# Kernel optimization log

Measured on AMD Instinct MI355X. Metric: run time of the kernel, lower is better.

The kernel has to match this reference:

```python
import jax, jax.numpy as jnp
import numpy as np

EPS = 1e-6
SIGMA = 0.1  # temperature for pseudo-LBS blend weights


def _quat_rotate(q, v):
    # q: [..., 4] (w, x, y, z) unit quaternions, v: [..., 3]
    qw, qv = q[..., :1], q[..., 1:]
    t = 2.0 * jnp.cross(qv, v)
    return v + qw * t + jnp.cross(qv, t)


def _pairwise_sqdist(a, b):
    # a: [n, d], b: [m, d] -> [n, m]
    return (jnp.sum(a * a, -1, keepdims=True)
            + jnp.sum(b * b, -1)[None, :]
            - 2.0 * (a @ b.T))


def setup_inputs() -> dict:
    N, K, F, V, J, P, M, H = 300000, 80, 64, 6890, 24, 64, 64, 128
    key = jax.random.key(0)
    ks = jax.random.split(key, 16)
    s = lambda i, shape: jax.random.normal(ks[i], shape, dtype=jnp.float32) * 0.05
    return {
        "xyz": jax.random.normal(ks[0], (N, 3), dtype=jnp.float32),
        "feature": jax.random.normal(ks[1], (N, F), dtype=jnp.float32),
        "centers": jax.random.normal(ks[2], (K, F), dtype=jnp.float32),
        "smpl_verts": jax.random.normal(ks[3], (V, 3), dtype=jnp.float32),
        "skinning_weights": jax.random.uniform(ks[4], (V, J), dtype=jnp.float32),
        "body_pose_feature": jax.random.normal(ks[5], (J, P), dtype=jnp.float32),
        "w_body": s(6, (P + F, M)),
        "b_body": jnp.zeros((M,), jnp.float32),
        "w_pos1": s(7, (3 + M, H)),
        "b_pos1": jnp.zeros((H,), jnp.float32),
        "w_pos2": s(8, (H, M)),
        "b_pos2": jnp.zeros((M,), jnp.float32),
        "w_rot": s(9, (M, 4)),
        "b_rot": jnp.zeros((4,), jnp.float32),
        "w_trans": s(10, (M, 3)),
        "b_trans": jnp.zeros((3,), jnp.float32),
    }


def reference(xyz, feature, centers, smpl_verts, skinning_weights,
              body_pose_feature, w_body, b_body, w_pos1, b_pos1,
              w_pos2, b_pos2, w_rot, b_rot, w_trans, b_trans):
    # ---- soft k-means: soft assignment of N points to K garment joints ----
    a = jax.nn.softmax(-_pairwise_sqdist(feature, centers), axis=-1)  # [N, K]
    cnt = a.sum(axis=0) + EPS                                          # [K]
    # weighted segment-reduce: c_assign^T @ xyz, diag(1/count) normalize
    joint_xyz = (a.T @ xyz) / cnt[:, None]      # [K, 3]
    joint_feat = (a.T @ feature) / cnt[:, None]  # [K, F] (cluster centers)

    # ---- KNN (k=1) skin-weight lookup against SMPL canonical verts ----
    idx = jnp.argmin(_pairwise_sqdist(joint_xyz, smpl_verts), axis=-1)  # [K]
    pts_W = skinning_weights[idx]                                        # [K, J]

    # ---- garment pose decoder ----
    body_feat = pts_W @ body_pose_feature                 # [K, P]
    g = jnp.concatenate([body_feat, joint_feat], axis=-1)  # [K, P+F]
    g = jax.nn.gelu(g @ w_body + b_body)                   # [K, M]
    lo, hi = smpl_verts.min(0), smpl_verts.max(0)
    xn = 2.0 * (joint_xyz - lo) / (hi - lo + EPS) - 1.0    # aabb sym-normalize
    h = jax.nn.relu(jnp.concatenate([xn, g], -1) @ w_pos1 + b_pos1)
    g2 = h @ w_pos2 + b_pos2                               # [K, M]
    q = g2 @ w_rot + b_rot
    q = q / (jnp.linalg.norm(q, axis=-1, keepdims=True) + EPS)  # [K, 4]
    t = g2 @ w_trans + b_trans                                   # [K, 3]

    # ---- pseudo-LBS: blend per-joint transforms back to N points ----
    w = jax.nn.softmax(-_pairwise_sqdist(xyz, joint_xyz) / SIGMA, axis=-1)  # [N, K]
    qb = w @ q
    qb = qb / (jnp.linalg.norm(qb, axis=-1, keepdims=True) + EPS)  # [N, 4]
    deformed_xyz = _quat_rotate(qb, xyz) + w @ t                    # [N, 3]
    return deformed_xyz
```

## Files before the change

### kernel.cpp

```cpp
#include <hip/hip_runtime.h>
#include <math.h>

#define N_PTS 300000
#define NJ 80
#define FDIM 64
#define VN 6890
#define NROUND 9375
#define GRID_A 256
#define TOTW 1024
#define SLOT_B 8704

typedef __attribute__((ext_vector_type(8))) short short8;
typedef __attribute__((ext_vector_type(4))) float f32x4;

union Frag { uint32_t u[4]; short8 v; };

__device__ __forceinline__ uint32_t packhi(float a, float b) {
  return (__float_as_uint(a) >> 16) | (__float_as_uint(b) & 0xFFFF0000u);
}
__device__ __forceinline__ uint32_t packlo(float a, float b) {
  float la = a - __uint_as_float(__float_as_uint(a) & 0xFFFF0000u);
  float lb = b - __uint_as_float(__float_as_uint(b) & 0xFFFF0000u);
  return packhi(la, lb);
}

#define DPPF(x, ctrl) __uint_as_float((uint32_t)__builtin_amdgcn_update_dpp( \
    0, (int)__float_as_uint(x), (ctrl), 0xF, 0xF, true))

__device__ __forceinline__ void gl16(const float* g, const void* l) {
  __builtin_amdgcn_global_load_lds(
      (const __attribute__((address_space(1))) void*)g,
      (__attribute__((address_space(3))) void*)l, 16, 0, 0);
}
__device__ __forceinline__ void gl4(const float* g, const void* l) {
  __builtin_amdgcn_global_load_lds(
      (const __attribute__((address_space(1))) void*)g,
      (__attribute__((address_space(3))) void*)l, 4, 0, 0);
}

__global__ __launch_bounds__(256, 2) void kA(
    const float* __restrict__ xyz, const float* __restrict__ feature,
    const float* __restrict__ centers, float* __restrict__ jacc,
    float* __restrict__ part)
{
  __shared__ __align__(16) unsigned char ring[4][3][SLOT_B];
  __shared__ ushort sChi[NJ][72];
  __shared__ ushort sClo[NJ][72];

  const int tid = threadIdx.x;
  const int w = tid >> 6;
  const int l = tid & 63;
  const int i = l & 15;
  const int g = l >> 4;
  const int gw = blockIdx.x * 4 + w;

  auto STAGE = [&](int st, int rs) {
    const float* fb = feature + (size_t)rs * 2048;
    unsigned char* base = &ring[w][st][0];
#pragma unroll
    for (int k = 0; k < 8; ++k) {
      const int lu = k * 64 + l;
      const int ptl = lu >> 4;
      const int gu = ptl * 16 + ((lu & 15) ^ (ptl & 7));
      gl16(fb + gu * 4, base + k * 1024);
    }
    const float* xb = xyz + (size_t)rs * 96;
#pragma unroll
    for (int k = 0; k < 2; ++k) {
      int fi = k * 64 + l; if (fi > 95) fi = 95;
      gl4(xb + fi, base + 8192 + k * 256);
    }
  };

  {
    int r1 = gw + TOTW; if (r1 > NROUND - 1) r1 = NROUND - 1;
    STAGE(0, gw);
    STAGE(1, r1);
  }

  for (int idx = tid; idx < NJ * FDIM; idx += 256) {
    float f = centers[idx];
    sChi[idx >> 6][idx & 63] = (ushort)(__float_as_uint(f) >> 16);
    float lo = f - __uint_as_float(__float_as_uint(f) & 0xFFFF0000u);
    sClo[idx >> 6][idx & 63] = (ushort)(__float_as_uint(lo) >> 16);
  }
  float cn[5];
#pragma unroll
  for (int nt = 0; nt < 5; ++nt) {
    float s = 0.f;
    const float* cp = centers + (size_t)(i + 16 * nt) * FDIM + 8 * g;
#pragma unroll
    for (int e = 0; e < 8; ++e) {
      float a0 = cp[e], a1 = cp[32 + e];
      s += a0 * a0 + a1 * a1;
    }
    s += __shfl_xor(s, 16);
    s += __shfl_xor(s, 32);
    cn[nt] = s;
  }
  __syncthreads();

  f32x4 acc2[5][5];
#pragma unroll
  for (int a = 0; a < 5; ++a)
#pragma unroll
    for (int b = 0; b < 5; ++b) acc2[a][b] = (f32x4){0.f, 0.f, 0.f, 0.f};

  int s3 = 0;
  for (int r = gw; r < NROUND; r += TOTW) {
    asm volatile("s_waitcnt vmcnt(10)" ::: "memory");
    __builtin_amdgcn_sched_barrier(0);
    {
      int rn = r + 2 * TOTW; if (rn > NROUND - 1) rn = NROUND - 1;
      int st = s3 + 2; if (st >= 3) st -= 3;
      STAGE(st, rn);
    }
    __builtin_amdgcn_sched_barrier(0);

    const float* F = (const float*)&ring[w][s3][0];
    const float* X = (const float*)&ring[w][s3][8192];

    Frag pA[5];
#pragma unroll
    for (int c = 0; c < 2; ++c) {
      f32x4 acc1[5];
#pragma unroll
      for (int nt = 0; nt < 5; ++nt) acc1[nt] = (f32x4){0.f, 0.f, 0.f, 0.f};

      const int ptl = 16 * c + i;
      const int m = ptl & 7;
#pragma unroll
      for (int ks = 0; ks < 2; ++ks) {
        const int j = 8 * ks + 2 * g;
        float4 va = *(const float4*)(F + ptl * 64 + ((j ^ m) << 2));
        float4 vb = *(const float4*)(F + ptl * 64 + (((j + 1) ^ m) << 2));
        Frag ah, al;
        ah.u[0] = packhi(va.x, va.y); ah.u[1] = packhi(va.z, va.w);
        ah.u[2] = packhi(vb.x, vb.y); ah.u[3] = packhi(vb.z, vb.w);
        al.u[0] = packlo(va.x, va.y); al.u[1] = packlo(va.z, va.w);
        al.u[2] = packlo(vb.x, vb.y); al.u[3] = packlo(vb.z, vb.w);
#pragma unroll
        for (int nt = 0; nt < 5; ++nt) {
          Frag bh, bl;
          *(uint4*)bh.u = *(const uint4*)&sChi[i + 16 * nt][32 * ks + 8 * g];
          *(uint4*)bl.u = *(const uint4*)&sClo[i + 16 * nt][32 * ks + 8 * g];
          acc1[nt] = __builtin_amdgcn_mfma_f32_16x16x32_bf16(ah.v, bh.v, acc1[nt], 0, 0, 0);
          acc1[nt] = __builtin_amdgcn_mfma_f32_16x16x32_bf16(al.v, bh.v, acc1[nt], 0, 0, 0);
          acc1[nt] = __builtin_amdgcn_mfma_f32_16x16x32_bf16(ah.v, bl.v, acc1[nt], 0, 0, 0);
        }
      }

      f32x4 e5[5];
#pragma unroll
      for (int nt = 0; nt < 5; ++nt)
#pragma unroll
        for (int rr = 0; rr < 4; ++rr) e5[nt][rr] = 2.f * acc1[nt][rr] - cn[nt];
      float rs[4];
#pragma unroll
      for (int rr = 0; rr < 4; ++rr) {
        float mm = e5[0][rr];
#pragma unroll
        for (int nt = 1; nt < 5; ++nt) mm = fmaxf(mm, e5[nt][rr]);
        mm = fmaxf(mm, DPPF(mm, 0xB1));
        mm = fmaxf(mm, DPPF(mm, 0x4E));
        mm = fmaxf(mm, DPPF(mm, 0x141));
        mm = fmaxf(mm, DPPF(mm, 0x140));
        float ss = 0.f;
#pragma unroll
        for (int nt = 0; nt < 5; ++nt) {
          float e = __expf(e5[nt][rr] - mm);
          e5[nt][rr] = e;
          ss += e;
        }
        ss += DPPF(ss, 0xB1);
        ss += DPPF(ss, 0x4E);
        ss += DPPF(ss, 0x141);
        ss += DPPF(ss, 0x140);
        rs[rr] = __builtin_amdgcn_rcpf(ss);
      }
#pragma unroll
      for (int nt = 0; nt < 5; ++nt) {
        pA[nt].u[2 * c + 0] = packhi(e5[nt][0] * rs[0], e5[nt][1] * rs[1]);
        pA[nt].u[2 * c + 1] = packhi(e5[nt][2] * rs[2], e5[nt][3] * rs[3]);
      }
    }

#pragma unroll
    for (int ct = 0; ct < 5; ++ct) {
      Frag B;
      float x[8];
      if (ct < 4) {
        const int d = 16 * ct + i, jd = d >> 2, db = d & 3;
#pragma unroll
        for (int n = 0; n < 8; ++n) {
          const int ptl = (n < 4) ? (4 * g + n) : (16 + 4 * g + (n - 4));
          x[n] = F[ptl * 64 + ((jd ^ (ptl & 7)) << 2) + db];
        }
      } else {
#pragma unroll
        for (int n = 0; n < 8; ++n) {
          const int ptl = (n < 4) ? (4 * g + n) : (16 + 4 * g + (n - 4));
          x[n] = (i < 3) ? X[ptl * 3 + i] : (i == 3 ? 1.f : 0.f);
        }
      }
      B.u[0] = packhi(x[0], x[1]); B.u[1] = packhi(x[2], x[3]);
      B.u[2] = packhi(x[4], x[5]); B.u[3] = packhi(x[6], x[7]);
#pragma unroll
      for (int nt = 0; nt < 5; ++nt)
        acc2[nt][ct] = __builtin_amdgcn_mfma_f32_16x16x32_bf16(pA[nt].v, B.v, acc2[nt][ct], 0, 0, 0);
    }

    s3 += 1; if (s3 >= 3) s3 -= 3;
  }

  asm volatile("s_waitcnt vmcnt(0)" ::: "memory");
  __syncthreads();
  float* sJ = (float*)&ring[0][0][0];
  for (int idx = tid; idx < 5440; idx += 256) sJ[idx] = 0.f;
  __syncthreads();
#pragma unroll
  for (int ww = 0; ww < 4; ++ww) {
    if (w == ww) {
#pragma unroll
      for (int nt = 0; nt < 5; ++nt)
#pragma unroll
        for (int ct = 0; ct < 5; ++ct) {
          if (ct < 4 || i < 4) {
            const int col = 16 * ct + i;
#pragma unroll
            for (int rr = 0; rr < 4; ++rr)
              sJ[(16 * nt + 4 * g + rr) * 68 + col] += acc2[nt][ct][rr];
          }
        }
    }
    __syncthreads();
  }
  if (part) {
    for (int idx = tid; idx < 5440; idx += 256)
      part[(size_t)blockIdx.x * 5440 + idx] = sJ[idx];
  } else {
    for (int idx = tid; idx < 5440; idx += 256)
      atomicAdd(&jacc[idx], sJ[idx]);
  }
}

__global__ __launch_bounds__(256) void kR(const float* __restrict__ part,
                                          float* __restrict__ jacc)
{
  const int bx = blockIdx.x;
  const int cg = bx % 22, sl = bx / 22;
  const int t = cg * 256 + threadIdx.x;
  if (t >= 5440) return;
  const int b0 = sl * (GRID_A / 16);
  float s0 = 0.f, s1 = 0.f, s2 = 0.f, s3 = 0.f;
  for (int b = b0; b < b0 + GRID_A / 16; b += 4) {
    s0 += part[(size_t)(b + 0) * 5440 + t];
    s1 += part[(size_t)(b + 1) * 5440 + t];
    s2 += part[(size_t)(b + 2) * 5440 + t];
    s3 += part[(size_t)(b + 3) * 5440 + t];
  }
  atomicAdd(&jacc[t], (s0 + s1) + (s2 + s3));
}

__global__ __launch_bounds__(64) void kB(
    const float* __restrict__ jacc, const float* __restrict__ smpl,
    const float* __restrict__ sw, const float* __restrict__ bpf,
    const float* __restrict__ w_body, const float* __restrict__ b_body,
    const float* __restrict__ w_pos1, const float* __restrict__ b_pos1,
    const float* __restrict__ w_pos2, const float* __restrict__ b_pos2,
    const float* __restrict__ w_rot,  const float* __restrict__ b_rot,
    const float* __restrict__ w_trans,const float* __restrict__ b_trans,
    float* __restrict__ jpack, float* __restrict__ qpack,
    float* __restrict__ tpack)
{
  const int k = blockIdx.x;
  const int l = threadIdx.x;
  __shared__ float gin[128];
  __shared__ float in2[67];
  __shared__ float h2[128];
  __shared__ float g2[64];
  __shared__ float q7[8];

  const float cnt = jacc[k*68 + 67] + 1e-6f;
  gin[64 + l] = jacc[k*68 + l] / cnt;
  const float jx = jacc[k*68 + 64] / cnt;
  const float jy = jacc[k*68 + 65] / cnt;
  const float jz = jacc[k*68 + 66] / cnt;

  float lo0 = 1e30f, lo1 = 1e30f, lo2 = 1e30f;
  float hi0 = -1e30f, hi1 = -1e30f, hi2 = -1e30f;
  float best = 1e30f; int bi = 0;
  for (int v = l; v < VN; v += 64) {
    float x = smpl[v*3], y = smpl[v*3+1], z = smpl[v*3+2];
    lo0 = fminf(lo0, x); hi0 = fmaxf(hi0, x);
    lo1 = fminf(lo1, y); hi1 = fmaxf(hi1, y);
    lo2 = fminf(lo2, z); hi2 = fmaxf(hi2, z);
    float dx = x - jx, dy = y - jy, dz = z - jz;
    float d = dx*dx + dy*dy + dz*dz;
    if (d < best) { best = d; bi = v; }
  }
#pragma unroll
  for (int m = 1; m < 64; m <<= 1) {
    lo0 = fminf(lo0, __shfl_xor(lo0, m));
    lo1 = fminf(lo1, __shfl_xor(lo1, m));
    lo2 = fminf(lo2, __shfl_xor(lo2, m));
    hi0 = fmaxf(hi0, __shfl_xor(hi0, m));
    hi1 = fmaxf(hi1, __shfl_xor(hi1, m));
    hi2 = fmaxf(hi2, __shfl_xor(hi2, m));
    float d2 = __shfl_xor(best, m); int i2 = __shfl_xor(bi, m);
    if (d2 < best || (d2 == best && i2 < bi)) { best = d2; bi = i2; }
  }

  {
    float s = 0.f;
    for (int j = 0; j < 24; ++j) s += sw[bi*24 + j] * bpf[j*64 + l];
    gin[l] = s;
  }
  if (l < 3) {
    float lo = (l == 0) ? lo0 : (l == 1) ? lo1 : lo2;
    float hi = (l == 0) ? hi0 : (l == 1) ? hi1 : hi2;
    float jc = (l == 0) ? jx : (l == 1) ? jy : jz;
    in2[l] = 2.f * (jc - lo) / (hi - lo + 1e-6f) - 1.f;
  }
  __syncthreads();

  {
    float s = b_body[l];
    for (int t = 0; t < 128; ++t) s += gin[t] * w_body[t*64 + l];
    float u = 0.7978845608028654f * (s + 0.044715f * s * s * s);
    float e = __expf(2.f * u);
    float th = 1.f - 2.f / (e + 1.f);
    in2[3 + l] = 0.5f * s * (1.f + th);
  }
  __syncthreads();

#pragma unroll
  for (int half = 0; half < 2; ++half) {
    const int m = l + 64*half;
    float s = b_pos1[m];
    for (int t = 0; t < 67; ++t) s += in2[t] * w_pos1[t*128 + m];
    h2[m] = fmaxf(s, 0.f);
  }
  __syncthreads();

  {
    float s = b_pos2[l];
    for (int t = 0; t < 128; ++t) s += h2[t] * w_pos2[t*64 + l];
    g2[l] = s;
  }
  __syncthreads();

  if (l < 4) {
    float s = b_rot[l];
    for (int t = 0; t < 64; ++t) s += g2[t] * w_rot[t*4 + l];
    q7[l] = s;
  } else if (l < 7) {
    const int j = l - 4;
    float s = b_trans[j];
    for (int t = 0; t < 64; ++t) s += g2[t] * w_trans[t*3 + j];
    q7[l] = s;
  }
  __syncthreads();
  if (l == 0) {
    float q0 = q7[0], q1 = q7[1], q2 = q7[2], q3 = q7[3];
    float rn = 1.f / (sqrtf(q0*q0 + q1*q1 + q2*q2 + q3*q3) + 1e-6f);
    *(float4*)&qpack[k*4] = make_float4(q0*rn, q1*rn, q2*rn, q3*rn);
    *(float4*)&tpack[k*4] = make_float4(q7[4], q7[5], q7[6], 0.f);
    *(float4*)&jpack[k*4] = make_float4(jx, jy, jz, jx*jx + jy*jy + jz*jz);
  }
}

__global__ __launch_bounds__(256) void kC(
    const float* __restrict__ xyz, const float* __restrict__ jpack,
    const float* __restrict__ qpack, const float* __restrict__ tpack,
    float* __restrict__ out)
{
  __shared__ float4 sj[NJ], sq[NJ], st[NJ];
  __shared__ float sxy[768];
  const int tid = threadIdx.x;
  const int pbase = blockIdx.x * 256;
  const int nval = min(256, N_PTS - pbase);
  const int cnt3 = nval * 3;

  if (tid < 80)        sj[tid]       = ((const float4*)jpack)[tid];
  else if (tid < 160)  sq[tid - 80]  = ((const float4*)qpack)[tid - 80];
  else if (tid < 240)  st[tid - 160] = ((const float4*)tpack)[tid - 160];
  for (int t = tid; t < cnt3; t += 256) sxy[t] = xyz[(size_t)pbase * 3 + t];
  __syncthreads();

  const bool valid = tid < nval;
  float x0 = 0.f, x1 = 0.f, x2 = 0.f;
  if (valid) { x0 = sxy[tid*3]; x1 = sxy[tid*3+1]; x2 = sxy[tid*3+2]; }
  __syncthreads();

  float lv[NJ];
  float m = -1e30f;
#pragma unroll
  for (int k = 0; k < NJ; ++k) {
    float4 j = sj[k];
    lv[k] = (2.f*(x0*j.x + x1*j.y + x2*j.z) - j.w) * 10.0f;
    m = fmaxf(m, lv[k]);
  }
  float s = 0.f;
  float qb0=0,qb1=0,qb2=0,qb3=0, tb0=0,tb1=0,tb2=0;
#pragma unroll
  for (int k = 0; k < NJ; ++k) {
    float e = __expf(lv[k] - m);
    s += e;
    float4 q = sq[k];
    float4 t = st[k];
    qb0 += e*q.x; qb1 += e*q.y; qb2 += e*q.z; qb3 += e*q.w;
    tb0 += e*t.x; tb1 += e*t.y; tb2 += e*t.z;
  }
  float rs = 1.f / s;
  qb0*=rs; qb1*=rs; qb2*=rs; qb3*=rs; tb0*=rs; tb1*=rs; tb2*=rs;
  float nrm = sqrtf(qb0*qb0+qb1*qb1+qb2*qb2+qb3*qb3) + 1e-6f;
  float rn = 1.f / nrm;
  float qw = qb0*rn, qx = qb1*rn, qy = qb2*rn, qz = qb3*rn;
  float t2x = 2.f*(qy*x2 - qz*x1);
  float t2y = 2.f*(qz*x0 - qx*x2);
  float t2z = 2.f*(qx*x1 - qy*x0);
  float cx = qy*t2z - qz*t2y;
  float cy = qz*t2x - qx*t2z;
  float cz = qx*t2y - qy*t2x;
  float r0 = x0 + qw*t2x + cx + tb0;
  float r1 = x1 + qw*t2y + cy + tb1;
  float r2 = x2 + qw*t2z + cz + tb2;

  if (valid) { sxy[tid*3] = r0; sxy[tid*3+1] = r1; sxy[tid*3+2] = r2; }
  __syncthreads();
  for (int t = tid; t < cnt3; t += 256) out[(size_t)pbase * 3 + t] = sxy[t];
}

extern "C" void kernel_launch(void* const* d_in, const int* in_sizes, int n_in,
                              void* d_out, int out_size, void* d_ws, size_t ws_size,
                              hipStream_t stream) {
  const float* xyz     = (const float*)d_in[0];
  const float* feature = (const float*)d_in[1];
  const float* centers = (const float*)d_in[2];
  const float* smpl    = (const float*)d_in[3];
  const float* sw      = (const float*)d_in[4];
  const float* bpf     = (const float*)d_in[5];
  const float* w_body  = (const float*)d_in[6];
  const float* b_body  = (const float*)d_in[7];
  const float* w_pos1  = (const float*)d_in[8];
  const float* b_pos1  = (const float*)d_in[9];
  const float* w_pos2  = (const float*)d_in[10];
  const float* b_pos2  = (const float*)d_in[11];
  const float* w_rot   = (const float*)d_in[12];
  const float* b_rot   = (const float*)d_in[13];
  const float* w_trans = (const float*)d_in[14];
  const float* b_trans = (const float*)d_in[15];
  float* out = (float*)d_out;

  float* ws    = (float*)d_ws;
  float* jacc  = ws;
  float* jpack = ws + 5440;
  float* qpack = ws + 5760;
  float* tpack = ws + 6080;
  float* part  = ws + 6400;

  const size_t need = (size_t)6400 + (size_t)GRID_A * 5440;
  const bool use_part = (ws_size / 4) >= need;
  float* part_arg = use_part ? part : nullptr;

  hipMemsetAsync(jacc, 0, 5440 * sizeof(float), stream);
  kA<<<dim3(GRID_A), dim3(256), 0, stream>>>(xyz, feature, centers, jacc, part_arg);
  if (use_part)
    kR<<<dim3(22 * 16), dim3(256), 0, stream>>>(part, jacc);
  kB<<<dim3(NJ), dim3(64), 0, stream>>>(jacc, smpl, sw, bpf,
                                        w_body, b_body, w_pos1, b_pos1,
                                        w_pos2, b_pos2, w_rot, b_rot,
                                        w_trans, b_trans, jpack, qpack, tpack);
  kC<<<dim3((N_PTS + 255) / 256), dim3(256), 0, stream>>>(xyz, jpack, qpack, tpack, out);
}
```

Measured before the change: 128.7 us.

## Widen kA to 8 waves with double buffering and fold reduction into kB

kA now runs 512 threads (8 waves) per block, so twice the rounds are in flight per block. The triple-buffered LDS ring becomes a double buffer, with the next stage issued at the top of each iteration. The first GEMM is reordered so both 16-point chunks share each B-fragment load. The separate kR reduction kernel and the memset are removed, and kB now sums the 256 per-block partials directly. The trade-off is higher register and LDS pressure per block, less prefetch depth, and a serial 256-way reduction inside each kB block.

```diff
diff --git a/kernel.cpp b/kernel.cpp
--- a/kernel.cpp
+++ b/kernel.cpp
@@ -7,7 +7,7 @@
 #define VN 6890
 #define NROUND 9375
 #define GRID_A 256
-#define TOTW 1024
+#define TOTW 2048
 #define SLOT_B 8704
 
 typedef __attribute__((ext_vector_type(8))) short short8;
@@ -38,12 +38,12 @@
       (__attribute__((address_space(3))) void*)l, 4, 0, 0);
 }
 
-__global__ __launch_bounds__(256, 2) void kA(
+__global__ __launch_bounds__(512, 2) void kA(
     const float* __restrict__ xyz, const float* __restrict__ feature,
     const float* __restrict__ centers, float* __restrict__ jacc,
     float* __restrict__ part)
 {
-  __shared__ __align__(16) unsigned char ring[4][3][SLOT_B];
+  __shared__ __align__(16) unsigned char ring[8][2][SLOT_B];
   __shared__ ushort sChi[NJ][72];
   __shared__ ushort sClo[NJ][72];
 
@@ -52,7 +52,7 @@
   const int l = tid & 63;
   const int i = l & 15;
   const int g = l >> 4;
-  const int gw = blockIdx.x * 4 + w;
+  const int gw = blockIdx.x * 8 + w;
 
   auto STAGE = [&](int st, int rs) {
     const float* fb = feature + (size_t)rs * 2048;
@@ -72,13 +72,9 @@
     }
   };
 
-  {
-    int r1 = gw + TOTW; if (r1 > NROUND - 1) r1 = NROUND - 1;
-    STAGE(0, gw);
-    STAGE(1, r1);
-  }
-
-  for (int idx = tid; idx < NJ * FDIM; idx += 256) {
+  STAGE(0, gw);
+
+  for (int idx = tid; idx < NJ * FDIM; idx += 512) {
     float f = centers[idx];
     sChi[idx >> 6][idx & 63] = (ushort)(__float_as_uint(f) >> 16);
     float lo = f - __uint_as_float(__float_as_uint(f) & 0xFFFF0000u);
@@ -106,55 +102,61 @@
 #pragma unroll
     for (int b = 0; b < 5; ++b) acc2[a][b] = (f32x4){0.f, 0.f, 0.f, 0.f};
 
-  int s3 = 0;
+  int s2 = 0;
   for (int r = gw; r < NROUND; r += TOTW) {
+    {
+      int rn = r + TOTW; if (rn > NROUND - 1) rn = NROUND - 1;
+      STAGE(s2 ^ 1, rn);
+    }
     asm volatile("s_waitcnt vmcnt(10)" ::: "memory");
     __builtin_amdgcn_sched_barrier(0);
-    {
-      int rn = r + 2 * TOTW; if (rn > NROUND - 1) rn = NROUND - 1;
-      int st = s3 + 2; if (st >= 3) st -= 3;
-      STAGE(st, rn);
-    }
-    __builtin_amdgcn_sched_barrier(0);
-
-    const float* F = (const float*)&ring[w][s3][0];
-    const float* X = (const float*)&ring[w][s3][8192];
-
-    Frag pA[5];
-#pragma unroll
-    for (int c = 0; c < 2; ++c) {
-      f32x4 acc1[5];
-#pragma unroll
-      for (int nt = 0; nt < 5; ++nt) acc1[nt] = (f32x4){0.f, 0.f, 0.f, 0.f};
-
-      const int ptl = 16 * c + i;
-      const int m = ptl & 7;
-#pragma unroll
-      for (int ks = 0; ks < 2; ++ks) {
+
+    const float* F = (const float*)&ring[w][s2][0];
+    const float* X = (const float*)&ring[w][s2][8192];
+
+    f32x4 acc1[2][5];
+#pragma unroll
+    for (int c = 0; c < 2; ++c)
+#pragma unroll
+      for (int nt = 0; nt < 5; ++nt) acc1[c][nt] = (f32x4){0.f, 0.f, 0.f, 0.f};
+
+#pragma unroll
+    for (int ks = 0; ks < 2; ++ks) {
+      Frag ah[2], al[2];
+#pragma unroll
+      for (int c = 0; c < 2; ++c) {
+        const int ptl = 16 * c + i;
+        const int m = ptl & 7;
         const int j = 8 * ks + 2 * g;
         float4 va = *(const float4*)(F + ptl * 64 + ((j ^ m) << 2));
         float4 vb = *(const float4*)(F + ptl * 64 + (((j + 1) ^ m) << 2));
-        Frag ah, al;
-        ah.u[0] = packhi(va.x, va.y); ah.u[1] = packhi(va.z, va.w);
-        ah.u[2] = packhi(vb.x, vb.y); ah.u[3] = packhi(vb.z, vb.w);
-        al.u[0] = packlo(va.x, va.y); al.u[1] = packlo(va.z, va.w);
-        al.u[2] = packlo(vb.x, vb.y); al.u[3] = packlo(vb.z, vb.w);
-#pragma unroll
-        for (int nt = 0; nt < 5; ++nt) {
-          Frag bh, bl;
-          *(uint4*)bh.u = *(const uint4*)&sChi[i + 16 * nt][32 * ks + 8 * g];
-          *(uint4*)bl.u = *(const uint4*)&sClo[i + 16 * nt][32 * ks + 8 * g];
-          acc1[nt] = __builtin_amdgcn_mfma_f32_16x16x32_bf16(ah.v, bh.v, acc1[nt], 0, 0, 0);
-          acc1[nt] = __builtin_amdgcn_mfma_f32_16x16x32_bf16(al.v, bh.v, acc1[nt], 0, 0, 0);
-          acc1[nt] = __builtin_amdgcn_mfma_f32_16x16x32_bf16(ah.v, bl.v, acc1[nt], 0, 0, 0);
+        ah[c].u[0] = packhi(va.x, va.y); ah[c].u[1] = packhi(va.z, va.w);
+        ah[c].u[2] = packhi(vb.x, vb.y); ah[c].u[3] = packhi(vb.z, vb.w);
+        al[c].u[0] = packlo(va.x, va.y); al[c].u[1] = packlo(va.z, va.w);
+        al[c].u[2] = packlo(vb.x, vb.y); al[c].u[3] = packlo(vb.z, vb.w);
+      }
+#pragma unroll
+      for (int nt = 0; nt < 5; ++nt) {
+        Frag bh, bl;
+        *(uint4*)bh.u = *(const uint4*)&sChi[i + 16 * nt][32 * ks + 8 * g];
+        *(uint4*)bl.u = *(const uint4*)&sClo[i + 16 * nt][32 * ks + 8 * g];
+#pragma unroll
+        for (int c = 0; c < 2; ++c) {
+          acc1[c][nt] = __builtin_amdgcn_mfma_f32_16x16x32_bf16(ah[c].v, bh.v, acc1[c][nt], 0, 0, 0);
+          acc1[c][nt] = __builtin_amdgcn_mfma_f32_16x16x32_bf16(al[c].v, bh.v, acc1[c][nt], 0, 0, 0);
+          acc1[c][nt] = __builtin_amdgcn_mfma_f32_16x16x32_bf16(ah[c].v, bl.v, acc1[c][nt], 0, 0, 0);
         }
       }
-
+    }
+
+    Frag pA[5];
+#pragma unroll
+    for (int c = 0; c < 2; ++c) {
       f32x4 e5[5];
 #pragma unroll
       for (int nt = 0; nt < 5; ++nt)
 #pragma unroll
-        for (int rr = 0; rr < 4; ++rr) e5[nt][rr] = 2.f * acc1[nt][rr] - cn[nt];
+        for (int rr = 0; rr < 4; ++rr) e5[nt][rr] = 2.f * acc1[c][nt][rr] - cn[nt];
       float rs[4];
 #pragma unroll
       for (int rr = 0; rr < 4; ++rr) {
@@ -210,16 +212,16 @@
         acc2[nt][ct] = __builtin_amdgcn_mfma_f32_16x16x32_bf16(pA[nt].v, B.v, acc2[nt][ct], 0, 0, 0);
     }
 
-    s3 += 1; if (s3 >= 3) s3 -= 3;
+    s2 ^= 1;
   }
 
   asm volatile("s_waitcnt vmcnt(0)" ::: "memory");
   __syncthreads();
   float* sJ = (float*)&ring[0][0][0];
-  for (int idx = tid; idx < 5440; idx += 256) sJ[idx] = 0.f;
-  __syncthreads();
-#pragma unroll
-  for (int ww = 0; ww < 4; ++ww) {
+  for (int idx = tid; idx < 5440; idx += 512) sJ[idx] = 0.f;
+  __syncthreads();
+#pragma unroll
+  for (int ww = 0; ww < 8; ++ww) {
     if (w == ww) {
 #pragma unroll
       for (int nt = 0; nt < 5; ++nt)
@@ -236,34 +238,17 @@
     __syncthreads();
   }
   if (part) {
-    for (int idx = tid; idx < 5440; idx += 256)
+    for (int idx = tid; idx < 5440; idx += 512)
       part[(size_t)blockIdx.x * 5440 + idx] = sJ[idx];
   } else {
-    for (int idx = tid; idx < 5440; idx += 256)
+    for (int idx = tid; idx < 5440; idx += 512)
       atomicAdd(&jacc[idx], sJ[idx]);
   }
 }
 
-__global__ __launch_bounds__(256) void kR(const float* __restrict__ part,
-                                          float* __restrict__ jacc)
-{
-  const int bx = blockIdx.x;
-  const int cg = bx % 22, sl = bx / 22;
-  const int t = cg * 256 + threadIdx.x;
-  if (t >= 5440) return;
-  const int b0 = sl * (GRID_A / 16);
-  float s0 = 0.f, s1 = 0.f, s2 = 0.f, s3 = 0.f;
-  for (int b = b0; b < b0 + GRID_A / 16; b += 4) {
-    s0 += part[(size_t)(b + 0) * 5440 + t];
-    s1 += part[(size_t)(b + 1) * 5440 + t];
-    s2 += part[(size_t)(b + 2) * 5440 + t];
-    s3 += part[(size_t)(b + 3) * 5440 + t];
-  }
-  atomicAdd(&jacc[t], (s0 + s1) + (s2 + s3));
-}
-
 __global__ __launch_bounds__(64) void kB(
-    const float* __restrict__ jacc, const float* __restrict__ smpl,
+    const float* __restrict__ jacc, const float* __restrict__ part,
+    const float* __restrict__ smpl,
     const float* __restrict__ sw, const float* __restrict__ bpf,
     const float* __restrict__ w_body, const float* __restrict__ b_body,
     const float* __restrict__ w_pos1, const float* __restrict__ b_pos1,
@@ -275,17 +260,42 @@
 {
   const int k = blockIdx.x;
   const int l = threadIdx.x;
+  __shared__ float sh68[68];
   __shared__ float gin[128];
   __shared__ float in2[67];
   __shared__ float h2[128];
   __shared__ float g2[64];
   __shared__ float q7[8];
 
-  const float cnt = jacc[k*68 + 67] + 1e-6f;
-  gin[64 + l] = jacc[k*68 + l] / cnt;
-  const float jx = jacc[k*68 + 64] / cnt;
-  const float jy = jacc[k*68 + 65] / cnt;
-  const float jz = jacc[k*68 + 66] / cnt;
+  if (part) {
+    float a0 = 0.f, a1 = 0.f, a2 = 0.f, a3 = 0.f;
+    float e0 = 0.f, e1 = 0.f, e2 = 0.f, e3 = 0.f;
+    const float* pk = part + k * 68;
+    for (int b = 0; b < GRID_A; b += 4) {
+      a0 += pk[(size_t)(b + 0) * 5440 + l];
+      a1 += pk[(size_t)(b + 1) * 5440 + l];
+      a2 += pk[(size_t)(b + 2) * 5440 + l];
+      a3 += pk[(size_t)(b + 3) * 5440 + l];
+      if (l < 4) {
+        e0 += pk[(size_t)(b + 0) * 5440 + 64 + l];
+        e1 += pk[(size_t)(b + 1) * 5440 + 64 + l];
+        e2 += pk[(size_t)(b + 2) * 5440 + 64 + l];
+        e3 += pk[(size_t)(b + 3) * 5440 + 64 + l];
+      }
+    }
+    sh68[l] = (a0 + a1) + (a2 + a3);
+    if (l < 4) sh68[64 + l] = (e0 + e1) + (e2 + e3);
+  } else {
+    sh68[l] = jacc[k * 68 + l];
+    if (l < 4) sh68[64 + l] = jacc[k * 68 + 64 + l];
+  }
+  __syncthreads();
+
+  const float cnt = sh68[67] + 1e-6f;
+  gin[64 + l] = sh68[l] / cnt;
+  const float jx = sh68[64] / cnt;
+  const float jy = sh68[65] / cnt;
+  const float jz = sh68[66] / cnt;
 
   float lo0 = 1e30f, lo1 = 1e30f, lo2 = 1e30f;
   float hi0 = -1e30f, hi1 = -1e30f, hi2 = -1e30f;
@@ -464,11 +474,9 @@
   const bool use_part = (ws_size / 4) >= need;
   float* part_arg = use_part ? part : nullptr;
 
-  hipMemsetAsync(jacc, 0, 5440 * sizeof(float), stream);
-  kA<<<dim3(GRID_A), dim3(256), 0, stream>>>(xyz, feature, centers, jacc, part_arg);
-  if (use_part)
-    kR<<<dim3(22 * 16), dim3(256), 0, stream>>>(part, jacc);
-  kB<<<dim3(NJ), dim3(64), 0, stream>>>(jacc, smpl, sw, bpf,
+  if (!use_part) hipMemsetAsync(jacc, 0, 5440 * sizeof(float), stream);
+  kA<<<dim3(GRID_A), dim3(512), 0, stream>>>(xyz, feature, centers, jacc, part_arg);
+  kB<<<dim3(NJ), dim3(64), 0, stream>>>(jacc, part_arg, smpl, sw, bpf,
                                         w_body, b_body, w_pos1, b_pos1,
                                         w_pos2, b_pos2, w_rot, b_rot,
                                         w_trans, b_trans, jpack, qpack, tpack);
```

New measurement: 147.4 us. +14.6%, slower.
